# Kernel optimization log

Measured on AMD Instinct MI355X. Metric: run time of the kernel, lower is better.

The kernel has to match this reference:

```python
import jax, jax.numpy as jnp
import numpy as np

A_MIN = 0.001
EPS = 1e-08


def setup_inputs() -> dict:
    key = jax.random.key(0)
    k1, k2, k3, k4 = jax.random.split(key, 4)
    B, O, I = 512, 1024, 512
    x = jax.random.normal(k1, (B, I), dtype=jnp.float32)
    translation = jax.random.uniform(k2, (O, I), dtype=jnp.float32, minval=-1.0, maxval=1.0)
    scale_raw = jax.random.uniform(k3, (O, I), dtype=jnp.float32, minval=-2.0, maxval=0.0)
    weights = jax.random.normal(k4, (O, I), dtype=jnp.float32) * (1.0 / np.sqrt(I))
    return {"x": x, "translation": translation, "scale_raw": scale_raw, "weights": weights}


def reference(x, translation, scale_raw, weights):
    # x: (B, I); params: (O, I)
    scale = A_MIN + jax.nn.softplus(scale_raw)  # (O, I)
    # s: (B, O, I) broadcast intermediate
    s = (x[:, None, :] - translation[None, :, :]) / (scale[None, :, :] + EPS)
    s2 = s * s
    wavelet = (1.0 - s2) * jnp.exp(-0.5 * s2)  # mexican hat
    y = jnp.einsum('oi,boi->bo', weights, wavelet)  # reduce over in_features
    return y
```

## Files before the change

kernel.cpp:

```cpp
#include <hip/hip_runtime.h>
#include <hip/hip_bf16.h>


#define WL_A_MIN 0.001f
#define WL_EPS   1e-8f

constexpr int WL_B = 512;
constexpr int WL_O = 1024;
constexpr int WL_I = 512;

constexpr int O_TILE = 16;
constexpr int B_TILE = 32;
constexpr int KC     = 64;

constexpr int PS = KC * 4 + 4;
constexpr int XS = B_TILE + 4;

#define WL_K    0.72134752044448170368f
#define WL_SQK  0.84932180553704583800f
#define WL_IK   1.38629436111989061883f
#define WL_L2E  1.44269504088896340736f
#define WL_LN2  0.69314718055994530942f

typedef float v2f __attribute__((ext_vector_type(2)));

__device__ __forceinline__ float fast_exp2(float a) {
#if __has_builtin(__builtin_amdgcn_exp2f)
    return __builtin_amdgcn_exp2f(a);
#else
    return exp2f(a);
#endif
}
__device__ __forceinline__ float fast_log2(float a) {
#if __has_builtin(__builtin_amdgcn_logf)
    return __builtin_amdgcn_logf(a);
#else
    return __log2f(a);
#endif
}
__device__ __forceinline__ float fast_rcp(float a) {
#if __has_builtin(__builtin_amdgcn_rcpf)
    return __builtin_amdgcn_rcpf(a);
#else
    return 1.0f / a;
#endif
}

__global__ __launch_bounds__(256, 4) void wl_fused(
    const float* __restrict__ x,
    const float* __restrict__ translation,
    const float* __restrict__ scale_raw,
    const float* __restrict__ weights,
    float* __restrict__ out)
{
    __shared__ float p_lds[O_TILE * PS];
    __shared__ float x_lds[KC * XS];

    const int tid    = threadIdx.x;
    const int ox     = tid & 15;
    const int bg     = tid >> 4;
    const int o_base = blockIdx.x * O_TILE;
    const int b_base = blockIdx.y * B_TILE;

    v2f acc = {0.0f, 0.0f};

    for (int kc = 0; kc < WL_I; kc += KC) {
        #pragma unroll
        for (int k = 0; k < 4; ++k) {
            int lin = k * 256 + tid;
            int o_l = lin >> 6;
            int i_l = lin & 63;
            int gi  = (o_base + o_l) * WL_I + kc + i_l;
            float t  = translation[gi];
            float sr = scale_raw[gi];
            float w  = weights[gi];
            float ex  = fast_exp2(sr * WL_L2E);
            float sp  = fast_log2(1.0f + ex) * WL_LN2;
            float inv = fast_rcp(WL_A_MIN + sp + WL_EPS);
            float inv_s = inv * WL_SQK;
            float4 pv = make_float4(-t * inv_s, inv_s, w, w * WL_IK);
            *reinterpret_cast<float4*>(&p_lds[o_l * PS + i_l * 4]) = pv;
        }
        {
            int b_r = tid & 31;
            int ig  = tid >> 5;
            const float4* xr = reinterpret_cast<const float4*>(
                &x[(b_base + b_r) * WL_I + kc + ig * 8]);
            float4 v0 = xr[0];
            float4 v1 = xr[1];
            int base = (ig * 8) * XS + b_r;
            x_lds[base + 0 * XS] = v0.x;
            x_lds[base + 1 * XS] = v0.y;
            x_lds[base + 2 * XS] = v0.z;
            x_lds[base + 3 * XS] = v0.w;
            x_lds[base + 4 * XS] = v1.x;
            x_lds[base + 5 * XS] = v1.y;
            x_lds[base + 6 * XS] = v1.z;
            x_lds[base + 7 * XS] = v1.w;
        }
        __syncthreads();

        const float* pr = &p_lds[ox * PS];

        #pragma unroll 8
        for (int i = 0; i < KC; ++i) {
            float4 p = *reinterpret_cast<const float4*>(&pr[i * 4]);
            v2f x2 = *reinterpret_cast<const v2f*>(&x_lds[i * XS + bg * 2]);
            v2f inv2 = {p.y, p.y};
            v2f nti2 = {p.x, p.x};
            v2f s  = __builtin_elementwise_fma(x2, inv2, nti2);
            v2f u  = s * s;
            v2f e  = {fast_exp2(-u.x), fast_exp2(-u.y)};
            v2f w2  = {p.z, p.z};
            acc = __builtin_elementwise_fma(w2, e, acc);
            v2f ue = u * e;
            v2f nw2 = {-p.w, -p.w};
            acc = __builtin_elementwise_fma(nw2, ue, acc);
        }
        __syncthreads();
    }

    const int o = o_base + ox;
    const int b = b_base + bg * 2;
    out[(b + 0) * WL_O + o] = acc.x;
    out[(b + 1) * WL_O + o] = acc.y;
}

extern "C" void kernel_launch(void* const* d_in, const int* in_sizes, int n_in,
                              void* d_out, int out_size, void* d_ws, size_t ws_size,
                              hipStream_t stream) {
    const float* x           = (const float*)d_in[0];
    const float* translation = (const float*)d_in[1];
    const float* scale_raw   = (const float*)d_in[2];
    const float* weights     = (const float*)d_in[3];
    float*       out         = (float*)d_out;

    wl_fused<<<dim3(WL_O / O_TILE, WL_B / B_TILE), dim3(256), 0, stream>>>(
        x, translation, scale_raw, weights, out);
}
```

Before: 113.4 us.

## Double batch tile so each thread computes four outputs

Raises the batch tile from 32 to 64 rows, so each thread now produces four batch outputs per o instead of two, using two packed accumulators. The per-(o,i) parameter preprocessing (softplus, reciprocal) and the parameter loads are amortized over twice as many batch rows, and the grid halves. The cost is more registers and a launch bound relaxed to 2 blocks per SM, which lowers occupancy. The main loop remains bound by the exp2 work.

```diff
diff --git a/kernel.cpp b/kernel.cpp
--- a/kernel.cpp
+++ b/kernel.cpp
@@ -10,13 +10,12 @@
 constexpr int WL_I = 512;
 
 constexpr int O_TILE = 16;
-constexpr int B_TILE = 32;
+constexpr int B_TILE = 64;
 constexpr int KC     = 64;
 
 constexpr int PS = KC * 4 + 4;
 constexpr int XS = B_TILE + 4;
 
-#define WL_K    0.72134752044448170368f
 #define WL_SQK  0.84932180553704583800f
 #define WL_IK   1.38629436111989061883f
 #define WL_L2E  1.44269504088896340736f
@@ -46,7 +45,7 @@
 #endif
 }
 
-__global__ __launch_bounds__(256, 4) void wl_fused(
+__global__ __launch_bounds__(256, 2) void wl_fused(
     const float* __restrict__ x,
     const float* __restrict__ translation,
     const float* __restrict__ scale_raw,
@@ -62,7 +61,8 @@
     const int o_base = blockIdx.x * O_TILE;
     const int b_base = blockIdx.y * B_TILE;
 
-    v2f acc = {0.0f, 0.0f};
+    v2f accA = {0.0f, 0.0f};
+    v2f accB = {0.0f, 0.0f};
 
     for (int kc = 0; kc < WL_I; kc += KC) {
         #pragma unroll
@@ -74,56 +74,63 @@
             float t  = translation[gi];
             float sr = scale_raw[gi];
             float w  = weights[gi];
-            float ex  = fast_exp2(sr * WL_L2E);
-            float sp  = fast_log2(1.0f + ex) * WL_LN2;
-            float inv = fast_rcp(WL_A_MIN + sp + WL_EPS);
+            float ex    = fast_exp2(sr * WL_L2E);
+            float sp    = fast_log2(1.0f + ex) * WL_LN2;
+            float inv   = fast_rcp(WL_A_MIN + sp + WL_EPS);
             float inv_s = inv * WL_SQK;
             float4 pv = make_float4(-t * inv_s, inv_s, w, w * WL_IK);
             *reinterpret_cast<float4*>(&p_lds[o_l * PS + i_l * 4]) = pv;
         }
         {
-            int b_r = tid & 31;
-            int ig  = tid >> 5;
-            const float4* xr = reinterpret_cast<const float4*>(
-                &x[(b_base + b_r) * WL_I + kc + ig * 8]);
-            float4 v0 = xr[0];
-            float4 v1 = xr[1];
-            int base = (ig * 8) * XS + b_r;
-            x_lds[base + 0 * XS] = v0.x;
-            x_lds[base + 1 * XS] = v0.y;
-            x_lds[base + 2 * XS] = v0.z;
-            x_lds[base + 3 * XS] = v0.w;
-            x_lds[base + 4 * XS] = v1.x;
-            x_lds[base + 5 * XS] = v1.y;
-            x_lds[base + 6 * XS] = v1.z;
-            x_lds[base + 7 * XS] = v1.w;
+            int b_r = tid & 63;
+            int seg = tid >> 6;
+            const float* xg = &x[(b_base + b_r) * WL_I + kc + seg * 16];
+            #pragma unroll
+            for (int q = 0; q < 4; ++q) {
+                float4 v = *reinterpret_cast<const float4*>(&xg[q * 4]);
+                int i0 = seg * 16 + q * 4;
+                x_lds[(i0 + 0) * XS + b_r] = v.x;
+                x_lds[(i0 + 1) * XS + b_r] = v.y;
+                x_lds[(i0 + 2) * XS + b_r] = v.z;
+                x_lds[(i0 + 3) * XS + b_r] = v.w;
+            }
         }
         __syncthreads();
 
         const float* pr = &p_lds[ox * PS];
 
-        #pragma unroll 8
+        #pragma unroll 4
         for (int i = 0; i < KC; ++i) {
-            float4 p = *reinterpret_cast<const float4*>(&pr[i * 4]);
-            v2f x2 = *reinterpret_cast<const v2f*>(&x_lds[i * XS + bg * 2]);
+            float4 p  = *reinterpret_cast<const float4*>(&pr[i * 4]);
+            float4 xq = *reinterpret_cast<const float4*>(&x_lds[i * XS + bg * 4]);
+            v2f nti2 = {p.x, p.x};
             v2f inv2 = {p.y, p.y};
-            v2f nti2 = {p.x, p.x};
-            v2f s  = __builtin_elementwise_fma(x2, inv2, nti2);
-            v2f u  = s * s;
-            v2f e  = {fast_exp2(-u.x), fast_exp2(-u.y)};
-            v2f w2  = {p.z, p.z};
-            acc = __builtin_elementwise_fma(w2, e, acc);
-            v2f ue = u * e;
-            v2f nw2 = {-p.w, -p.w};
-            acc = __builtin_elementwise_fma(nw2, ue, acc);
+            v2f w2   = {p.z, p.z};
+            v2f nk2  = {-p.w, -p.w};
+            v2f xa = {xq.x, xq.y};
+            v2f xb = {xq.z, xq.w};
+            v2f sa = __builtin_elementwise_fma(xa, inv2, nti2);
+            v2f sb = __builtin_elementwise_fma(xb, inv2, nti2);
+            v2f ua = sa * sa;
+            v2f ub = sb * sb;
+            v2f ea = {fast_exp2(-ua.x), fast_exp2(-ua.y)};
+            v2f eb = {fast_exp2(-ub.x), fast_exp2(-ub.y)};
+            accA = __builtin_elementwise_fma(w2, ea, accA);
+            accB = __builtin_elementwise_fma(w2, eb, accB);
+            v2f uea = ua * ea;
+            v2f ueb = ub * eb;
+            accA = __builtin_elementwise_fma(nk2, uea, accA);
+            accB = __builtin_elementwise_fma(nk2, ueb, accB);
         }
         __syncthreads();
     }
 
     const int o = o_base + ox;
-    const int b = b_base + bg * 2;
-    out[(b + 0) * WL_O + o] = acc.x;
-    out[(b + 1) * WL_O + o] = acc.y;
+    const int b = b_base + bg * 4;
+    out[(b + 0) * WL_O + o] = accA.x;
+    out[(b + 1) * WL_O + o] = accA.y;
+    out[(b + 2) * WL_O + o] = accB.x;
+    out[(b + 3) * WL_O + o] = accB.y;
 }
 
 extern "C" void kernel_launch(void* const* d_in, const int* in_sizes, int n_in,
```

Result: no change. 114.5 us (+1.0%).
